# Performance work log

Measured on AMD Instinct MI355X. Metric: run time of the kernel, lower is better.

The kernel has to match this reference:

```python
import jax, jax.numpy as jnp
import numpy as np

HID = 1024
HEADS = 16
HEAD_DIM = HID // HEADS


def setup_inputs() -> dict:
    key = jax.random.key(0)
    ks = jax.random.split(key, 11)
    s = 1.0 / np.sqrt(HID)
    return {
        "query": jax.random.normal(ks[0], (4, 2048, HID), jnp.float32),
        "key": jax.random.normal(ks[1], (4, 2048, HID), jnp.float32),
        "value": jax.random.normal(ks[2], (4, 2048, HID), jnp.float32),
        "wq": jax.random.normal(ks[3], (HID, HID), jnp.float32) * s,
        "bq": jnp.zeros((HID,), jnp.float32),
        "wk": jax.random.normal(ks[4], (HID, HID), jnp.float32) * s,
        "bk": jnp.zeros((HID,), jnp.float32),
        "wv": jax.random.normal(ks[5], (HID, HID), jnp.float32) * s,
        "bv": jnp.zeros((HID,), jnp.float32),
        "wo": jax.random.normal(ks[6], (HID, HID), jnp.float32) * s,
        "bo": jnp.zeros((HID,), jnp.float32),
    }


def reference(query, key, value, wq, bq, wk, bk, wv, bv, wo, bo):
    b, s, _ = query.shape
    scale = jnp.sqrt(jnp.asarray(HEAD_DIM, query.dtype))
    # linear projections; weights stored as [in, out]
    Q = (query @ wq + bq).reshape(b, s, HEADS, HEAD_DIM).transpose(0, 2, 1, 3)
    K = (key @ wk + bk).reshape(b, s, HEADS, HEAD_DIM).transpose(0, 2, 1, 3)
    V = (value @ wv + bv).reshape(b, s, HEADS, HEAD_DIM).transpose(0, 2, 1, 3)
    energy = jnp.einsum('bhqd,bhkd->bhqk', Q, K) / scale  # [B,H,S,S]
    attention = jax.nn.softmax(energy, axis=-1)  # dropout p=0 -> identity
    x = jnp.einsum('bhqk,bhkd->bhqd', attention, V)
    x = x.transpose(0, 2, 1, 3).reshape(b, s, HID)
    return x @ wo + bo
```

## Files before the change

### kernel.cpp

```cpp
#include <hip/hip_runtime.h>
#include <hip/hip_bf16.h>

#define B_   4
#define S_   2048
#define HID_ 1024
#define H_   16
#define D_   64
#define M_   (B_ * S_)

typedef __attribute__((ext_vector_type(8)))  short bf16x8;
typedef __attribute__((ext_vector_type(4)))  float f32x4;
typedef __attribute__((ext_vector_type(16))) float f32x16;

#define GAS __attribute__((address_space(1)))
#define LAS __attribute__((address_space(3)))

__device__ __forceinline__ unsigned short f2bf(float f) {
    union { float f; unsigned int u; } x; x.f = f;
    unsigned int u = x.u;
    return (unsigned short)((u + 0x7fffu + ((u >> 16) & 1u)) >> 16);
}

__global__ __launch_bounds__(256)
void prep(const float* __restrict__ q, const float* __restrict__ k, const float* __restrict__ v,
          unsigned short* __restrict__ oq, unsigned short* __restrict__ ok,
          unsigned short* __restrict__ ov,
          const float* __restrict__ w0, const float* __restrict__ w1,
          const float* __restrict__ w2, const float* __restrict__ w3,
          unsigned short* __restrict__ t0, unsigned short* __restrict__ t1,
          unsigned short* __restrict__ t2, unsigned short* __restrict__ t3) {
    __shared__ float t[32][33];
    const int tid = threadIdx.x;
    if (blockIdx.x < 12288) {
        const int sel = blockIdx.x >> 12;
        const int i = (blockIdx.x & 4095) * 256 + tid;
        const float* in = (sel == 0) ? q : (sel == 1) ? k : v;
        unsigned short* out = (sel == 0) ? oq : (sel == 1) ? ok : ov;
        const f32x4 a = ((const f32x4*)in)[i * 2];
        const f32x4 b = ((const f32x4*)in)[i * 2 + 1];
        bf16x8 w;
#pragma unroll
        for (int j = 0; j < 4; j++) { w[j] = (short)f2bf(a[j]); w[4 + j] = (short)f2bf(b[j]); }
        ((bf16x8*)out)[i] = w;
    } else {
        const int tb = blockIdx.x - 12288;
        const int z = tb >> 10, rem = tb & 1023;
        const int bx = (rem & 31) * 32, by = (rem >> 5) * 32;
        const int tx = tid & 31, ty = tid >> 5;
        const float* w = (z == 0) ? w0 : (z == 1) ? w1 : (z == 2) ? w2 : w3;
        unsigned short* o = (z == 0) ? t0 : (z == 1) ? t1 : (z == 2) ? t2 : t3;
#pragma unroll
        for (int i = 0; i < 4; i++)
            t[ty + i * 8][tx] = w[(size_t)(by + ty + i * 8) * HID_ + bx + tx];
        __syncthreads();
#pragma unroll
        for (int i = 0; i < 4; i++)
            o[(size_t)(bx + ty + i * 8) * HID_ + by + tx] = f2bf(t[tx][ty + i * 8]);
    }
}

__global__ __launch_bounds__(256, 5)
void gemm_qkv(const unsigned short* __restrict__ aq, const unsigned short* __restrict__ ak,
              const unsigned short* __restrict__ av, const unsigned short* __restrict__ wqkvT,
              const float* __restrict__ bq, const float* __restrict__ bk,
              const float* __restrict__ bv, unsigned short* __restrict__ Qp,
              unsigned short* __restrict__ Kp, unsigned short* __restrict__ Vt, float cvt) {
    constexpr int BK = 32;
    constexpr int NT = HID_ / BK;
    __shared__ unsigned short smem[2][8192];

    const int tid  = threadIdx.x;
    const int lane = tid & 63;
    const int wave = tid >> 6;
    const int quad = lane >> 4;
    const int col  = lane & 15;
    const int wr   = (wave & 1) * 64;
    const int wc   = (wave >> 1) * 64;

    const int lb = blockIdx.x + gridDim.x * blockIdx.y;
    const int r8 = lb & 7, qq = lb >> 3;
    const int bx = r8 * 8 + (qq & 7);
    const int by = qq >> 3;
    const int m0   = bx * 128;
    const int third = by >> 3;
    const int n0l   = (by & 7) * 128;
    const bool vmode = (third == 2);

    const unsigned short* act = (third == 0) ? aq : (third == 1) ? ak : av;
    const float* bias = (third == 0) ? bq : (third == 1) ? bk : bv;
    unsigned short* outp = (third == 0) ? Qp : (third == 1) ? Kp : Vt;
    const float oscale = (third == 0) ? cvt : 1.f;

    const int grow = wave * 16 + (lane >> 2);
    const int gcol = (lane & 3) * 8;
    const unsigned short* wgp = wqkvT + (size_t)(third * HID_ + n0l + grow) * HID_ + gcol;
    const unsigned short* agp = act + (size_t)(m0 + grow) * HID_ + gcol;
    const unsigned short* rgp = vmode ? agp : wgp;
    const unsigned short* cgp = vmode ? wgp : agp;

    auto stage = [&](int buf, int kt) {
        unsigned short* as_ = &smem[buf][wave * 512];
        unsigned short* bs_ = &smem[buf][4096 + wave * 512];
        __builtin_amdgcn_global_load_lds((const GAS unsigned int*)(rgp + kt),
                                         (LAS unsigned int*)as_, 16, 0, 0);
        __builtin_amdgcn_global_load_lds((const GAS unsigned int*)(rgp + kt + (size_t)64 * HID_),
                                         (LAS unsigned int*)(as_ + 2048), 16, 0, 0);
        __builtin_amdgcn_global_load_lds((const GAS unsigned int*)(cgp + kt),
                                         (LAS unsigned int*)bs_, 16, 0, 0);
        __builtin_amdgcn_global_load_lds((const GAS unsigned int*)(cgp + kt + (size_t)64 * HID_),
                                         (LAS unsigned int*)(bs_ + 2048), 16, 0, 0);
    };

    f32x4 zero; zero[0] = 0.f; zero[1] = 0.f; zero[2] = 0.f; zero[3] = 0.f;
    f32x4 acc[4][4];
#pragma unroll
    for (int ri = 0; ri < 4; ri++)
#pragma unroll
        for (int ci = 0; ci < 4; ci++) acc[ri][ci] = zero;

    stage(0, 0);
    __syncthreads();

    for (int t = 0; t < NT; ++t) {
        const int cur = t & 1;
        if (t + 1 < NT) stage(cur ^ 1, (t + 1) * BK);
        const unsigned short* Asc = smem[cur];
        const unsigned short* Bsc = smem[cur] + 4096;
        bf16x8 af[4], cf[4];
#pragma unroll
        for (int i = 0; i < 4; i++) af[i] = *(const bf16x8*)&Asc[(wr + i * 16 + col) * BK + quad * 8];
#pragma unroll
        for (int i = 0; i < 4; i++) cf[i] = *(const bf16x8*)&Bsc[(wc + i * 16 + col) * BK + quad * 8];
#pragma unroll
        for (int ri = 0; ri < 4; ri++)
#pragma unroll
            for (int ci = 0; ci < 4; ci++)
                acc[ri][ci] = __builtin_amdgcn_mfma_f32_16x16x32_bf16(af[ri], cf[ci], acc[ri][ci], 0, 0, 0);
        __syncthreads();
    }

    unsigned short* RB = &smem[0][0];
#pragma unroll
    for (int ph = 0; ph < 2; ph++) {
        if ((wave >> 1) == ph) {
#pragma unroll
            for (int ri = 0; ri < 4; ri++) {
                f32x4 bv4;
                if (!vmode) bv4 = *(const f32x4*)&bias[n0l + wr + ri * 16 + quad * 4];
#pragma unroll
                for (int ci = 0; ci < 4; ci++) {
                    float b0, b1, b2, b3;
                    if (!vmode) { b0 = bv4[0]; b1 = bv4[1]; b2 = bv4[2]; b3 = bv4[3]; }
                    else { b0 = b1 = b2 = b3 = bias[n0l + wc + ci * 16 + col]; }
                    const unsigned int u0 = f2bf((acc[ri][ci][0] + b0) * oscale);
                    const unsigned int u1 = f2bf((acc[ri][ci][1] + b1) * oscale);
                    const unsigned int u2 = f2bf((acc[ri][ci][2] + b2) * oscale);
                    const unsigned int u3 = f2bf((acc[ri][ci][3] + b3) * oscale);
                    uint2 w; w.x = u0 | (u1 << 16); w.y = u2 | (u3 << 16);
                    *(uint2*)&RB[(ci * 16 + col) * 136 + wr + ri * 16 + quad * 4] = w;
                }
            }
        }
        __syncthreads();
#pragma unroll
        for (int it = 0; it < 4; it++) {
            const int c   = it * 256 + tid;
            const int row = c >> 4, ch = c & 15;
            const bf16x8 v = *(const bf16x8*)&RB[row * 136 + ch * 8];
            if (!vmode) {
                const int n = n0l + ch * 8;
                const int h = n >> 6, d = n & 63;
                const int m = m0 + ph * 64 + row;
                *(bf16x8*)&outp[(((size_t)(m >> 11) * H_ + h) * S_ + (m & 2047)) * D_ + d] = v;
            } else {
                const int m = m0 + ch * 8;
                const int n = n0l + ph * 64 + row;
                const int h = n >> 6, d = n & 63;
                *(bf16x8*)&outp[(((size_t)(m >> 11) * H_ + h) * D_ + d) * S_ + (m & 2047)] = v;
            }
        }
        __syncthreads();
    }
}

__global__ __launch_bounds__(256, 4)
void gemm_o(const unsigned short* __restrict__ A, const unsigned short* __restrict__ Bt,
            const float* __restrict__ bias, float* __restrict__ outp) {
    constexpr int BK = 32;
    constexpr int NT = HID_ / BK;
    __shared__ float smemf[64 * 132];
    unsigned short* sb = (unsigned short*)smemf;

    const int tid  = threadIdx.x;
    const int lane = tid & 63;
    const int wave = tid >> 6;
    const int quad = lane >> 4;
    const int col  = lane & 15;
    const int wn   = (wave >> 1) * 64;
    const int wm   = (wave & 1) * 32;

    const int lb = blockIdx.x + gridDim.x * blockIdx.y;
    const int r8 = lb & 7, qq = lb >> 3;
    const int m0  = (r8 * 16 + (qq & 15)) * 64;
    const int n0l = (qq >> 4) * 128;

    const int grow = wave * 16 + (lane >> 2);
    const int gcol = (lane & 3) * 8;
    const unsigned short* agp = A + (size_t)(m0 + grow) * HID_ + gcol;
    const unsigned short* wgp = Bt + (size_t)(n0l + grow) * HID_ + gcol;

    auto stage = [&](int buf, int kt) {
        unsigned short* as_ = sb + buf * 6144 + wave * 512;
        unsigned short* bs_ = sb + buf * 6144 + 4096 + wave * 512;
        __builtin_amdgcn_global_load_lds((const GAS unsigned int*)(wgp + kt),
                                         (LAS unsigned int*)as_, 16, 0, 0);
        __builtin_amdgcn_global_load_lds((const GAS unsigned int*)(wgp + kt + (size_t)64 * HID_),
                                         (LAS unsigned int*)(as_ + 2048), 16, 0, 0);
        __builtin_amdgcn_global_load_lds((const GAS unsigned int*)(agp + kt),
                                         (LAS unsigned int*)bs_, 16, 0, 0);
    };

    f32x4 zero; zero[0] = 0.f; zero[1] = 0.f; zero[2] = 0.f; zero[3] = 0.f;
    f32x4 acc[4][2];
#pragma unroll
    for (int ri = 0; ri < 4; ri++)
#pragma unroll
        for (int ci = 0; ci < 2; ci++) acc[ri][ci] = zero;

    stage(0, 0);
    __syncthreads();

    for (int t = 0; t < NT; ++t) {
        const int cur = t & 1;
        if (t + 1 < NT) stage(cur ^ 1, (t + 1) * BK);
        const unsigned short* Asc = sb + cur * 6144;
        const unsigned short* Bsc = Asc + 4096;
        bf16x8 wf[4], af[2];
#pragma unroll
        for (int i = 0; i < 4; i++) wf[i] = *(const bf16x8*)&Asc[(wn + i * 16 + col) * BK + quad * 8];
#pragma unroll
        for (int i = 0; i < 2; i++) af[i] = *(const bf16x8*)&Bsc[(wm + i * 16 + col) * BK + quad * 8];
#pragma unroll
        for (int ri = 0; ri < 4; ri++)
#pragma unroll
            for (int ci = 0; ci < 2; ci++)
                acc[ri][ci] = __builtin_amdgcn_mfma_f32_16x16x32_bf16(wf[ri], af[ci], acc[ri][ci], 0, 0, 0);
        __syncthreads();
    }

#pragma unroll
    for (int ri = 0; ri < 4; ri++) {
        const f32x4 bv4 = *(const f32x4*)&bias[n0l + wn + ri * 16 + quad * 4];
#pragma unroll
        for (int ci = 0; ci < 2; ci++) {
            f32x4 v;
#pragma unroll
            for (int i = 0; i < 4; i++) v[i] = acc[ri][ci][i] + bv4[i];
            *(f32x4*)&smemf[(wm + ci * 16 + col) * 132 + wn + ri * 16 + quad * 4] = v;
        }
    }
    __syncthreads();
#pragma unroll
    for (int it = 0; it < 8; it++) {
        const int c   = it * 256 + tid;
        const int row = c >> 5, ch = c & 31;
        const f32x4 v = *(const f32x4*)&smemf[row * 132 + ch * 4];
        *(f32x4*)&outp[(size_t)(m0 + row) * HID_ + n0l + ch * 4] = v;
    }
}

__global__ __launch_bounds__(256, 4)
void attn_k(const unsigned short* __restrict__ Qp, const unsigned short* __restrict__ Kp,
            const unsigned short* __restrict__ Vt, unsigned short* __restrict__ Xc) {
    constexpr int LT = 72;
    constexpr int NT = S_ / 64;
    __shared__ unsigned short Ks[2][64 * LT];
    __shared__ unsigned short Vs[2][64 * LT];

    const int tid  = threadIdx.x;
    const int lane = tid & 63;
    const int wave = tid >> 6;
    const int l31  = lane & 31;
    const int hw   = lane >> 5;

    const int lb = blockIdx.x + gridDim.x * blockIdx.y;
    const int r8 = lb & 7, qq = lb >> 3;
    const int bh = r8 + 8 * (qq >> 4);
    const int q0 = (qq & 15) * 128 + wave * 32;

    const unsigned short* Qb = Qp + (size_t)bh * S_ * D_;
    const unsigned short* Kb = Kp + (size_t)bh * S_ * D_;
    const unsigned short* Vb = Vt + (size_t)bh * D_ * S_;

    bf16x8 qf[4];
#pragma unroll
    for (int ks = 0; ks < 4; ks++)
        qf[ks] = *(const bf16x8*)&Qb[(q0 + l31) * D_ + ks * 16 + hw * 8];

    f32x16 o[2];
#pragma unroll
    for (int t = 0; t < 2; t++)
#pragma unroll
        for (int i = 0; i < 16; i++) o[t][i] = 0.f;
    float lpart = 0.f;

    const int srow = tid >> 3;
    const int seg  = (tid & 7) * 8;
    bf16x8 kr[2], vr[2];

#pragma unroll
    for (int it = 0; it < 2; it++) {
        const int row = it * 32 + srow;
        kr[it] = *(const bf16x8*)&Kb[(size_t)row * D_ + seg];
        vr[it] = *(const bf16x8*)&Vb[(size_t)row * S_ + seg];
    }
#pragma unroll
    for (int it = 0; it < 2; it++) {
        const int row = it * 32 + srow;
        *(bf16x8*)&Ks[0][row * LT + seg] = kr[it];
        *(bf16x8*)&Vs[0][row * LT + seg] = vr[it];
    }
#pragma unroll
    for (int it = 0; it < 2; it++) {
        const int row = it * 32 + srow;
        kr[it] = *(const bf16x8*)&Kb[(size_t)(64 + row) * D_ + seg];
        vr[it] = *(const bf16x8*)&Vb[(size_t)row * S_ + 64 + seg];
    }
    __syncthreads();

    for (int t = 0; t < NT; ++t) {
        const int cur = t & 1;

        f32x16 e0, e1;
#pragma unroll
        for (int i = 0; i < 16; i++) { e0[i] = 0.f; e1[i] = 0.f; }
        __builtin_amdgcn_s_setprio(1);
#pragma unroll
        for (int ks = 0; ks < 4; ks++) {
            const bf16x8 a0 = *(const bf16x8*)&Ks[cur][(l31) * LT + ks * 16 + hw * 8];
            const bf16x8 a1 = *(const bf16x8*)&Ks[cur][(32 + l31) * LT + ks * 16 + hw * 8];
            e0 = __builtin_amdgcn_mfma_f32_32x32x16_bf16(a0, qf[ks], e0, 0, 0, 0);
            e1 = __builtin_amdgcn_mfma_f32_32x32x16_bf16(a1, qf[ks], e1, 0, 0, 0);
        }
        __builtin_amdgcn_s_setprio(0);

        auto smpv = [&](const f32x16& e, int g) {
            unsigned int ulo[4], uhi[4];
#pragma unroll
            for (int grp = 0; grp < 4; grp++) {
                const float p0 = __builtin_amdgcn_exp2f(e[grp * 4 + 0]);
                const float p1 = __builtin_amdgcn_exp2f(e[grp * 4 + 1]);
                const float p2 = __builtin_amdgcn_exp2f(e[grp * 4 + 2]);
                const float p3 = __builtin_amdgcn_exp2f(e[grp * 4 + 3]);
                lpart += (p0 + p1) + (p2 + p3);
                asm("v_cvt_pk_bf16_f32 %0, %1, %2" : "=v"(ulo[grp]) : "v"(p0), "v"(p1));
                asm("v_cvt_pk_bf16_f32 %0, %1, %2" : "=v"(uhi[grp]) : "v"(p2), "v"(p3));
            }
#pragma unroll
            for (int sub = 0; sub < 2; sub++) {
                unsigned int w0 = ulo[2 * sub], w2 = ulo[2 * sub + 1];
                unsigned int w1 = uhi[2 * sub], w3 = uhi[2 * sub + 1];
                asm("v_permlane32_swap_b32 %0, %1" : "+v"(w0), "+v"(w2));
                asm("v_permlane32_swap_b32 %0, %1" : "+v"(w1), "+v"(w3));
                union { unsigned int u[4]; bf16x8 v; } pf;
                pf.u[0] = w0; pf.u[1] = w1; pf.u[2] = w2; pf.u[3] = w3;
                const int ks = g * 2 + sub;
                const bf16x8 vf0 = *(const bf16x8*)&Vs[cur][(l31) * LT + ks * 16 + hw * 8];
                const bf16x8 vf1 = *(const bf16x8*)&Vs[cur][(32 + l31) * LT + ks * 16 + hw * 8];
                __builtin_amdgcn_s_setprio(1);
                o[0] = __builtin_amdgcn_mfma_f32_32x32x16_bf16(vf0, pf.v, o[0], 0, 0, 0);
                o[1] = __builtin_amdgcn_mfma_f32_32x32x16_bf16(vf1, pf.v, o[1], 0, 0, 0);
                __builtin_amdgcn_s_setprio(0);
            }
        };
        smpv(e0, 0);
        smpv(e1, 1);

        if (t + 1 < NT) {
#pragma unroll
            for (int it = 0; it < 2; it++) {
                const int row = it * 32 + srow;
                *(bf16x8*)&Ks[cur ^ 1][row * LT + seg] = kr[it];
                *(bf16x8*)&Vs[cur ^ 1][row * LT + seg] = vr[it];
            }
            if (t + 2 < NT) {
                const int c0 = (t + 2) * 64;
#pragma unroll
                for (int it = 0; it < 2; it++) {
                    const int row = it * 32 + srow;
                    kr[it] = *(const bf16x8*)&Kb[(size_t)(c0 + row) * D_ + seg];
                    vr[it] = *(const bf16x8*)&Vb[(size_t)row * S_ + c0 + seg];
                }
            }
        }
        __syncthreads();
    }

    float l = lpart;
    l += __shfl_xor(l, 32);
    const float inv = 1.f / l;

    const int b = bh >> 4, h = bh & 15;
    const int s = q0 + l31;
    unsigned short* xp = &Xc[((size_t)(b * S_ + s)) * HID_ + h * D_];
#pragma unroll
    for (int t = 0; t < 2; t++)
#pragma unroll
        for (int grp = 0; grp < 4; grp++) {
            const unsigned int u0 = f2bf(o[t][grp * 4 + 0] * inv);
            const unsigned int u1 = f2bf(o[t][grp * 4 + 1] * inv);
            const unsigned int u2 = f2bf(o[t][grp * 4 + 2] * inv);
            const unsigned int u3 = f2bf(o[t][grp * 4 + 3] * inv);
            uint2 w; w.x = u0 | (u1 << 16); w.y = u2 | (u3 << 16);
            *(uint2*)&xp[t * 32 + grp * 8 + hw * 4] = w;
        }
}

extern "C" void kernel_launch(void* const* d_in, const int* in_sizes, int n_in,
                              void* d_out, int out_size, void* d_ws, size_t ws_size,
                              hipStream_t stream) {
    (void)in_sizes; (void)n_in; (void)out_size; (void)ws_size;
    const float* query = (const float*)d_in[0];
    const float* key   = (const float*)d_in[1];
    const float* value = (const float*)d_in[2];
    const float* wq    = (const float*)d_in[3];
    const float* bq    = (const float*)d_in[4];
    const float* wk    = (const float*)d_in[5];
    const float* bk    = (const float*)d_in[6];
    const float* wv    = (const float*)d_in[7];
    const float* bv    = (const float*)d_in[8];
    const float* wo    = (const float*)d_in[9];
    const float* bo    = (const float*)d_in[10];
    float* out = (float*)d_out;

    unsigned short* ws  = (unsigned short*)d_ws;
    const size_t WSZ = (size_t)HID_ * HID_;
    const size_t TSZ = (size_t)M_ * HID_;
    unsigned short* wqkvT = ws;
    unsigned short* woT = ws + 3 * WSZ;
    unsigned short* Qp  = woT + WSZ;
    unsigned short* Kp  = Qp + TSZ;
    unsigned short* Vt  = Kp + TSZ;
    unsigned short* Xc  = Vt + TSZ;
    unsigned short* Xb  = Xc + TSZ;

    const float cvt = 0.125f * 1.44269504f;

    prep<<<16384, 256, 0, stream>>>(
        query, key, value, Xc, Xb, Xb + TSZ,
        wq, wk, wv, wo, wqkvT, wqkvT + WSZ, wqkvT + 2 * WSZ, woT);

    gemm_qkv<<<dim3(M_ / 128, 24), 256, 0, stream>>>(
        Xc, Xb, Xb + TSZ, wqkvT, bq, bk, bv, Qp, Kp, Vt, cvt);

    attn_k<<<dim3(S_ / 128, B_ * H_), 256, 0, stream>>>(Qp, Kp, Vt, Xc);

    gemm_o<<<dim3(M_ / 64, 8), 256, 0, stream>>>(Xc, woT, bo, out);
}
```

Baseline: 336.5 us.

## Fuse fp32-to-bf16 activation cast into QKV GEMM operand loading

Removes the separate pass that converted query/key/value from fp32 to bf16. The QKV GEMM now loads fp32 activations into registers, converts them with packed bf16 conversion instructions, and writes them to shared memory after the MFMA block. Weights still go through direct global-to-LDS loads. This saves a full read and write of the bf16 activation copies, at the cost of twice the activation bytes read inside the GEMM, extra registers (occupancy hint lowered from 5 to 4), and register-staged rather than async loads.

```diff
diff --git a/kernel.cpp b/kernel.cpp
--- a/kernel.cpp
+++ b/kernel.cpp
@@ -21,47 +21,27 @@
     return (unsigned short)((u + 0x7fffu + ((u >> 16) & 1u)) >> 16);
 }
 
-__global__ __launch_bounds__(256)
-void prep(const float* __restrict__ q, const float* __restrict__ k, const float* __restrict__ v,
-          unsigned short* __restrict__ oq, unsigned short* __restrict__ ok,
-          unsigned short* __restrict__ ov,
-          const float* __restrict__ w0, const float* __restrict__ w1,
-          const float* __restrict__ w2, const float* __restrict__ w3,
-          unsigned short* __restrict__ t0, unsigned short* __restrict__ t1,
-          unsigned short* __restrict__ t2, unsigned short* __restrict__ t3) {
+__global__ void transpose_cast(const float* __restrict__ w0, const float* __restrict__ w1,
+                               const float* __restrict__ w2, const float* __restrict__ w3,
+                               unsigned short* __restrict__ o0, unsigned short* __restrict__ o1,
+                               unsigned short* __restrict__ o2, unsigned short* __restrict__ o3) {
     __shared__ float t[32][33];
-    const int tid = threadIdx.x;
-    if (blockIdx.x < 12288) {
-        const int sel = blockIdx.x >> 12;
-        const int i = (blockIdx.x & 4095) * 256 + tid;
-        const float* in = (sel == 0) ? q : (sel == 1) ? k : v;
-        unsigned short* out = (sel == 0) ? oq : (sel == 1) ? ok : ov;
-        const f32x4 a = ((const f32x4*)in)[i * 2];
-        const f32x4 b = ((const f32x4*)in)[i * 2 + 1];
-        bf16x8 w;
-#pragma unroll
-        for (int j = 0; j < 4; j++) { w[j] = (short)f2bf(a[j]); w[4 + j] = (short)f2bf(b[j]); }
-        ((bf16x8*)out)[i] = w;
-    } else {
-        const int tb = blockIdx.x - 12288;
-        const int z = tb >> 10, rem = tb & 1023;
-        const int bx = (rem & 31) * 32, by = (rem >> 5) * 32;
-        const int tx = tid & 31, ty = tid >> 5;
-        const float* w = (z == 0) ? w0 : (z == 1) ? w1 : (z == 2) ? w2 : w3;
-        unsigned short* o = (z == 0) ? t0 : (z == 1) ? t1 : (z == 2) ? t2 : t3;
-#pragma unroll
-        for (int i = 0; i < 4; i++)
-            t[ty + i * 8][tx] = w[(size_t)(by + ty + i * 8) * HID_ + bx + tx];
-        __syncthreads();
-#pragma unroll
-        for (int i = 0; i < 4; i++)
-            o[(size_t)(bx + ty + i * 8) * HID_ + by + tx] = f2bf(t[tx][ty + i * 8]);
-    }
-}
-
-__global__ __launch_bounds__(256, 5)
-void gemm_qkv(const unsigned short* __restrict__ aq, const unsigned short* __restrict__ ak,
-              const unsigned short* __restrict__ av, const unsigned short* __restrict__ wqkvT,
+    const float* w = (blockIdx.z == 0) ? w0 : (blockIdx.z == 1) ? w1 : (blockIdx.z == 2) ? w2 : w3;
+    unsigned short* o = (blockIdx.z == 0) ? o0 : (blockIdx.z == 1) ? o1 : (blockIdx.z == 2) ? o2 : o3;
+    const int tx = threadIdx.x, ty = threadIdx.y;
+    const int bx = blockIdx.x * 32, by = blockIdx.y * 32;
+#pragma unroll
+    for (int i = 0; i < 4; i++)
+        t[ty + i * 8][tx] = w[(size_t)(by + ty + i * 8) * HID_ + bx + tx];
+    __syncthreads();
+#pragma unroll
+    for (int i = 0; i < 4; i++)
+        o[(size_t)(bx + ty + i * 8) * HID_ + by + tx] = f2bf(t[tx][ty + i * 8]);
+}
+
+__global__ __launch_bounds__(256, 4)
+void gemm_qkv(const float* __restrict__ qf32, const float* __restrict__ kf32,
+              const float* __restrict__ vf32, const unsigned short* __restrict__ wqkvT,
               const float* __restrict__ bq, const float* __restrict__ bk,
               const float* __restrict__ bv, unsigned short* __restrict__ Qp,
               unsigned short* __restrict__ Kp, unsigned short* __restrict__ Vt, float cvt) {
@@ -86,7 +66,7 @@
     const int n0l   = (by & 7) * 128;
     const bool vmode = (third == 2);
 
-    const unsigned short* act = (third == 0) ? aq : (third == 1) ? ak : av;
+    const float* act = (third == 0) ? qf32 : (third == 1) ? kf32 : vf32;
     const float* bias = (third == 0) ? bq : (third == 1) ? bk : bv;
     unsigned short* outp = (third == 0) ? Qp : (third == 1) ? Kp : Vt;
     const float oscale = (third == 0) ? cvt : 1.f;
@@ -94,21 +74,36 @@
     const int grow = wave * 16 + (lane >> 2);
     const int gcol = (lane & 3) * 8;
     const unsigned short* wgp = wqkvT + (size_t)(third * HID_ + n0l + grow) * HID_ + gcol;
-    const unsigned short* agp = act + (size_t)(m0 + grow) * HID_ + gcol;
-    const unsigned short* rgp = vmode ? agp : wgp;
-    const unsigned short* cgp = vmode ? wgp : agp;
-
-    auto stage = [&](int buf, int kt) {
-        unsigned short* as_ = &smem[buf][wave * 512];
-        unsigned short* bs_ = &smem[buf][4096 + wave * 512];
-        __builtin_amdgcn_global_load_lds((const GAS unsigned int*)(rgp + kt),
-                                         (LAS unsigned int*)as_, 16, 0, 0);
-        __builtin_amdgcn_global_load_lds((const GAS unsigned int*)(rgp + kt + (size_t)64 * HID_),
-                                         (LAS unsigned int*)(as_ + 2048), 16, 0, 0);
-        __builtin_amdgcn_global_load_lds((const GAS unsigned int*)(cgp + kt),
-                                         (LAS unsigned int*)bs_, 16, 0, 0);
-        __builtin_amdgcn_global_load_lds((const GAS unsigned int*)(cgp + kt + (size_t)64 * HID_),
-                                         (LAS unsigned int*)(bs_ + 2048), 16, 0, 0);
+    const float* agp = act + (size_t)(m0 + grow) * HID_ + gcol;
+
+    auto stage_w = [&](int buf, int kt) {
+        unsigned short* dst = &smem[buf][(vmode ? 4096 : 0) + wave * 512];
+        __builtin_amdgcn_global_load_lds((const GAS unsigned int*)(wgp + kt),
+                                         (LAS unsigned int*)dst, 16, 0, 0);
+        __builtin_amdgcn_global_load_lds((const GAS unsigned int*)(wgp + kt + (size_t)64 * HID_),
+                                         (LAS unsigned int*)(dst + 2048), 16, 0, 0);
+    };
+
+    f32x4 ar[4];
+    auto load_act = [&](int kt) {
+        ar[0] = *(const f32x4*)(agp + kt);
+        ar[1] = *(const f32x4*)(agp + kt + 4);
+        ar[2] = *(const f32x4*)(agp + kt + (size_t)64 * HID_);
+        ar[3] = *(const f32x4*)(agp + kt + (size_t)64 * HID_ + 4);
+    };
+    auto write_act = [&](int buf) {
+        unsigned short* dst = &smem[buf][(vmode ? 0 : 4096) + wave * 512 + lane * 8];
+        union { unsigned int u[4]; bf16x8 v; } c0, c1;
+        asm("v_cvt_pk_bf16_f32 %0, %1, %2" : "=v"(c0.u[0]) : "v"(ar[0][0]), "v"(ar[0][1]));
+        asm("v_cvt_pk_bf16_f32 %0, %1, %2" : "=v"(c0.u[1]) : "v"(ar[0][2]), "v"(ar[0][3]));
+        asm("v_cvt_pk_bf16_f32 %0, %1, %2" : "=v"(c0.u[2]) : "v"(ar[1][0]), "v"(ar[1][1]));
+        asm("v_cvt_pk_bf16_f32 %0, %1, %2" : "=v"(c0.u[3]) : "v"(ar[1][2]), "v"(ar[1][3]));
+        asm("v_cvt_pk_bf16_f32 %0, %1, %2" : "=v"(c1.u[0]) : "v"(ar[2][0]), "v"(ar[2][1]));
+        asm("v_cvt_pk_bf16_f32 %0, %1, %2" : "=v"(c1.u[1]) : "v"(ar[2][2]), "v"(ar[2][3]));
+        asm("v_cvt_pk_bf16_f32 %0, %1, %2" : "=v"(c1.u[2]) : "v"(ar[3][0]), "v"(ar[3][1]));
+        asm("v_cvt_pk_bf16_f32 %0, %1, %2" : "=v"(c1.u[3]) : "v"(ar[3][2]), "v"(ar[3][3]));
+        *(bf16x8*)dst = c0.v;
+        *(bf16x8*)(dst + 2048) = c1.v;
     };
 
     f32x4 zero; zero[0] = 0.f; zero[1] = 0.f; zero[2] = 0.f; zero[3] = 0.f;
@@ -118,12 +113,17 @@
 #pragma unroll
         for (int ci = 0; ci < 4; ci++) acc[ri][ci] = zero;
 
-    stage(0, 0);
+    stage_w(0, 0);
+    load_act(0);
+    write_act(0);
     __syncthreads();
 
     for (int t = 0; t < NT; ++t) {
         const int cur = t & 1;
-        if (t + 1 < NT) stage(cur ^ 1, (t + 1) * BK);
+        if (t + 1 < NT) {
+            stage_w(cur ^ 1, (t + 1) * BK);
+            load_act((t + 1) * BK);
+        }
         const unsigned short* Asc = smem[cur];
         const unsigned short* Bsc = smem[cur] + 4096;
         bf16x8 af[4], cf[4];
@@ -136,6 +136,7 @@
 #pragma unroll
             for (int ci = 0; ci < 4; ci++)
                 acc[ri][ci] = __builtin_amdgcn_mfma_f32_16x16x32_bf16(af[ri], cf[ci], acc[ri][ci], 0, 0, 0);
+        if (t + 1 < NT) write_act(cur ^ 1);
         __syncthreads();
     }
 
@@ -442,16 +443,14 @@
     unsigned short* Kp  = Qp + TSZ;
     unsigned short* Vt  = Kp + TSZ;
     unsigned short* Xc  = Vt + TSZ;
-    unsigned short* Xb  = Xc + TSZ;
 
     const float cvt = 0.125f * 1.44269504f;
 
-    prep<<<16384, 256, 0, stream>>>(
-        query, key, value, Xc, Xb, Xb + TSZ,
+    transpose_cast<<<dim3(32, 32, 4), dim3(32, 8), 0, stream>>>(
         wq, wk, wv, wo, wqkvT, wqkvT + WSZ, wqkvT + 2 * WSZ, woT);
 
     gemm_qkv<<<dim3(M_ / 128, 24), 256, 0, stream>>>(
-        Xc, Xb, Xb + TSZ, wqkvT, bq, bk, bv, Qp, Kp, Vt, cvt);
+        query, key, value, wqkvT, bq, bk, bv, Qp, Kp, Vt, cvt);
 
     attn_k<<<dim3(S_ / 128, B_ * H_), 256, 0, stream>>>(Qp, Kp, Vt, Xc);
 
```

Result: slower. 347.3 us (+3.2%).
